# Kernel tuning notes

Measured on AMD Instinct MI355X. Metric: run time of the kernel, lower is better.

The kernel has to match this reference:

```python
import jax, jax.numpy as jnp
import numpy as np

D_MODEL = 2048
NUM_HEADS = 32
D_HEAD = D_MODEL // NUM_HEADS
L = 2048


def setup_inputs() -> dict:
    key = jax.random.key(0)
    ks = jax.random.split(key, 9)
    s = 0.02  # init scale
    return {
        "X": jax.random.normal(ks[0], (L, D_MODEL), dtype=jnp.float32),
        "Wq_w": jax.random.normal(ks[1], (D_MODEL, D_MODEL), jnp.float32) * s,
        "Wq_b": jax.random.normal(ks[2], (D_MODEL,), jnp.float32) * s,
        "Wk_w": jax.random.normal(ks[3], (D_MODEL, D_MODEL), jnp.float32) * s,
        "Wk_b": jax.random.normal(ks[4], (D_MODEL,), jnp.float32) * s,
        "Wv_w": jax.random.normal(ks[5], (D_MODEL, D_MODEL), jnp.float32) * s,
        "Wv_b": jax.random.normal(ks[6], (D_MODEL,), jnp.float32) * s,
        "Wo_w": jax.random.normal(ks[7], (D_MODEL, D_MODEL), jnp.float32) * s,
        "Wo_b": jax.random.normal(ks[8], (D_MODEL,), jnp.float32) * s,
    }


def reference(X, Wq_w, Wq_b, Wk_w, Wk_b, Wv_w, Wv_b, Wo_w, Wo_b):
    # torch.nn.Linear: y = x @ W.T + b
    seq = X.shape[0]
    Q = (X @ Wq_w.T + Wq_b).reshape(seq, D_HEAD, NUM_HEADS)  # (L, d, h)
    K = (X @ Wk_w.T + Wk_b).reshape(seq, D_HEAD, NUM_HEADS)
    V = (X @ Wv_w.T + Wv_b).reshape(seq, D_HEAD, NUM_HEADS)
    # scores[l, m, h] = sum_d Q[l,d,h] * K[m,d,h]; note scale is sqrt(d_model),
    # faithful to the source (not sqrt(d_head)).
    scores = jnp.einsum('ldh,mdh->lmh', Q, K) / jnp.sqrt(jnp.float32(D_MODEL))
    attn = jax.nn.softmax(scores, axis=1)  # softmax over key axis m
    out = jnp.einsum('lmh,mdh->ldh', attn, V).reshape(seq, D_MODEL)
    return out @ Wo_w.T + Wo_b
```

## Files before the change

kernel.cpp:

```cpp
#include <hip/hip_runtime.h>
#include <hip/hip_bf16.h>
#include <stdint.h>
#include <stddef.h>

#define L_SEQ   2048
#define DM      2048
#define NH      32
#define DH      64
#define QSCALE  0.02209708691207961f
#define QS2     0.0318793579f
#define MAT_N   (L_SEQ * DM)

typedef __bf16  bf16x8 __attribute__((ext_vector_type(8)));
typedef float   f32x4  __attribute__((ext_vector_type(4)));
typedef __hip_bfloat16 bf16;

#if __has_builtin(__builtin_amdgcn_exp2f)
#define EXP2F(x) __builtin_amdgcn_exp2f(x)
#else
#define EXP2F(x) __expf((x) * 0.6931471805599453f)
#endif

__device__ __forceinline__ void gl_lds16(const bf16* g, bf16* l) {
    __builtin_amdgcn_global_load_lds(
        (const __attribute__((address_space(1))) unsigned int*)g,
        (__attribute__((address_space(3))) unsigned int*)l,
        16, 0, 0);
}

__device__ __forceinline__ void conv8s(const float* src, bf16* dst, int i, float sc) {
    float4 a = *(const float4*)(src + i);
    float4 b = *(const float4*)(src + i + 4);
    union { bf16 h[8]; uint4 u; } pk;
    pk.h[0] = __float2bfloat16(a.x * sc); pk.h[1] = __float2bfloat16(a.y * sc);
    pk.h[2] = __float2bfloat16(a.z * sc); pk.h[3] = __float2bfloat16(a.w * sc);
    pk.h[4] = __float2bfloat16(b.x * sc); pk.h[5] = __float2bfloat16(b.y * sc);
    pk.h[6] = __float2bfloat16(b.z * sc); pk.h[7] = __float2bfloat16(b.w * sc);
    *(uint4*)(dst + i) = pk.u;
}

__global__ __launch_bounds__(256)
void convert4_kernel(const float* __restrict__ s0, const float* __restrict__ s1,
                     const float* __restrict__ s2, const float* __restrict__ s3,
                     bf16* __restrict__ d0, bf16* __restrict__ d1,
                     bf16* __restrict__ d2, bf16* __restrict__ d3)
{
    const float* s; bf16* d; float sc = 1.0f;
    switch (blockIdx.y) {
        case 0:  s = s0; d = d0; break;
        case 1:  s = s1; d = d1; sc = QS2; break;
        case 2:  s = s2; d = d2; break;
        default: s = s3; d = d3; break;
    }
    const int i = (blockIdx.x * 256 + threadIdx.x) * 8;
    conv8s(s, d, i, sc);
}

__global__ __launch_bounds__(256)
void convert_wo_perm_kernel(const float* __restrict__ s, bf16* __restrict__ d)
{
    const int t   = blockIdx.x * 256 + threadIdx.x;
    const int row = t >> 8;
    const int k0  = (t & 255) * 8;
    const float* sr = s + (size_t)row * DM;
    union { bf16 h[8]; uint4 u; } pk;
#pragma unroll
    for (int j = 0; j < 8; ++j) {
        const int kp = k0 + j;
        const int k  = ((kp & 63) << 5) | (kp >> 6);
        pk.h[j] = __float2bfloat16(sr[k]);
    }
    *(uint4*)(d + (size_t)row * DM + k0) = pk.u;
}

__global__ __launch_bounds__(512)
void qkv8_gemm_kernel(const bf16* __restrict__ Xb,
                      const bf16* __restrict__ Wq, const float* __restrict__ bq,
                      const bf16* __restrict__ Wk, const float* __restrict__ bk,
                      const bf16* __restrict__ Wv, const float* __restrict__ bv,
                      bf16* __restrict__ Qws, bf16* __restrict__ Kws, bf16* __restrict__ Vws,
                      const float* __restrict__ WoSrc, bf16* __restrict__ WobDst)
{
    __shared__ bf16 lds[2 * 32768];

    const int bid = blockIdx.x;
    const int tid  = threadIdx.x;

    if (bid >= 192) {
        const int t = (bid - 192) * 512 + tid;
        const int row = t >> 4;
        const int k0base = (t & 15) * 128;
        const float* sr = WoSrc + (size_t)row * DM;
        bf16* dr = WobDst + (size_t)row * DM;
        for (int i = 0; i < 16; ++i) {
            const int k0 = k0base + i * 8;
            union { bf16 h[8]; uint4 u; } pk;
#pragma unroll
            for (int j = 0; j < 8; ++j) {
                const int kp = k0 + j;
                const int k  = ((kp & 63) << 5) | (kp >> 6);
                pk.h[j] = __float2bfloat16(sr[k]);
            }
            *(uint4*)(dr + k0) = pk.u;
        }
        return;
    }

    const int mt  = bid & 7;
    const int nt  = bid >> 3;
    const int m0  = mt << 8;
    const int ng0 = nt << 8;
    const int z   = ng0 >> 11;
    const int n0  = ng0 & 2047;
    const bf16*  W    = (z == 0) ? Wq : (z == 1) ? Wk : Wv;
    const float* bias = (z == 0) ? bq : (z == 1) ? bk : bv;

    const int lane = tid & 63;
    const int wave = tid >> 6;
    const int wm   = wave >> 2;
    const int wn   = wave & 3;
    const int grp8 = (lane >> 4) * 8;
    const int grp4 = (lane >> 4) * 4;
    const int l15  = lane & 15;
    const int axor = (l15 & 7) << 3;

    const int scol = ((tid & 7) * 8) ^ (((tid >> 3) & 7) << 3);
    const bf16* gb[8];
    int loff[8];
#pragma unroll
    for (int e = 0; e < 8; ++e) {
        const int hh  = e >> 1;
        const int row = (e & 1) * 64 + (tid >> 3);
        loff[e] = hh * 8192 + (e & 1) * 4096 + tid * 8;
        if (hh < 2) {
            gb[e] = Xb + (size_t)(m0 + hh * 128 + row) * DM + scol;
        } else {
            const int nn   = n0 + (hh - 2) * 128 + row;
            const int brow = ((nn & 63) << 5) | (nn >> 6);
            gb[e] = W + (size_t)brow * DM + scol;
        }
    }

    const bool swap  = (z == 2);
    const int  aside = swap ? 16384 : 0;
    const int  bside = swap ? 0 : 16384;
    const bf16* fa0 = lds + aside + wm * 8192 + l15 * 64;
    const bf16* fb0 = lds + bside + (wn >> 1) * 8192 + ((wn & 1) * 64 + l15) * 64;

    f32x4 acc[8][4];
    const f32x4 zero = {0.f, 0.f, 0.f, 0.f};
#pragma unroll
    for (int i = 0; i < 8; ++i)
#pragma unroll
        for (int j = 0; j < 4; ++j) acc[i][j] = zero;

#pragma unroll
    for (int e = 0; e < 8; ++e) gl_lds16(gb[e],      lds + loff[e]);
#pragma unroll
    for (int e = 0; e < 8; ++e) gl_lds16(gb[e] + 64, lds + 32768 + loff[e]);
    asm volatile("s_waitcnt vmcnt(8)" ::: "memory");
    asm volatile("s_barrier" ::: "memory");

    for (int t = 0; t < 32; ++t) {
        const int cb = (t & 1) << 15;
        const bf16* fa = fa0 + cb;
        const bf16* fb = fb0 + cb;
        const int c0 = grp8 ^ axor;
        const int c1 = (32 + grp8) ^ axor;

        bf16x8 af[8], bfr[4];
#pragma unroll
        for (int i = 0; i < 8; ++i) af[i] = *(const bf16x8*)(fa + i * 1024 + c0);
#pragma unroll
        for (int j = 0; j < 4; ++j) bfr[j] = *(const bf16x8*)(fb + j * 1024 + c0);
        asm volatile("s_barrier" ::: "memory");
        __builtin_amdgcn_s_setprio(1);
#pragma unroll
        for (int i = 0; i < 8; ++i)
#pragma unroll
            for (int j = 0; j < 4; ++j)
                acc[i][j] = __builtin_amdgcn_mfma_f32_16x16x32_bf16(af[i], bfr[j], acc[i][j], 0, 0, 0);
        __builtin_amdgcn_s_setprio(0);

#pragma unroll
        for (int i = 0; i < 8; ++i) af[i] = *(const bf16x8*)(fa + i * 1024 + c1);
#pragma unroll
        for (int j = 0; j < 4; ++j) bfr[j] = *(const bf16x8*)(fb + j * 1024 + c1);
        asm volatile("s_waitcnt lgkmcnt(0)" ::: "memory");
        asm volatile("s_barrier" ::: "memory");
        if (t + 2 < 32) {
            const int kb2 = (t + 2) << 6;
#pragma unroll
            for (int e = 0; e < 8; ++e)
                gl_lds16(gb[e] + kb2, lds + cb + loff[e]);
            asm volatile("s_waitcnt vmcnt(8)" ::: "memory");
        } else if (t == 30) {
            asm volatile("s_waitcnt vmcnt(0)" ::: "memory");
        }
        __builtin_amdgcn_s_setprio(1);
#pragma unroll
        for (int i = 0; i < 8; ++i)
#pragma unroll
            for (int j = 0; j < 4; ++j)
                acc[i][j] = __builtin_amdgcn_mfma_f32_16x16x32_bf16(af[i], bfr[j], acc[i][j], 0, 0, 0);
        __builtin_amdgcn_s_setprio(0);
        asm volatile("s_barrier" ::: "memory");
    }

    if (z == 0) {
#pragma unroll
        for (int j = 0; j < 4; ++j) {
            const int np = n0 + wn * 64 + j * 16 + l15;
            const float bb = bias[((np & 63) << 5) | (np >> 6)] * QS2;
            const size_t base = ((size_t)(np >> 6) * L_SEQ) * DH + (np & 63);
#pragma unroll
            for (int i = 0; i < 8; ++i)
#pragma unroll
                for (int r = 0; r < 4; ++r) {
                    const int m = m0 + wm * 128 + i * 16 + grp4 + r;
                    Qws[base + (size_t)m * DH] = __float2bfloat16(acc[i][j][r] + bb);
                }
        }
    } else if (z == 1) {
#pragma unroll
        for (int j = 0; j < 4; ++j) {
            const int np = n0 + wn * 64 + j * 16 + l15;
            const float bb = bias[((np & 63) << 5) | (np >> 6)];
            const size_t base = ((size_t)(np >> 6) * L_SEQ) * DH + (np & 63);
#pragma unroll
            for (int i = 0; i < 8; ++i)
#pragma unroll
                for (int r = 0; r < 4; ++r) {
                    const int m = m0 + wm * 128 + i * 16 + grp4 + r;
                    Kws[base + (size_t)m * DH] = __float2bfloat16(acc[i][j][r] + bb);
                }
        }
    } else {
#pragma unroll
        for (int i = 0; i < 8; ++i)
#pragma unroll
            for (int r = 0; r < 4; ++r) {
                const int np = n0 + wm * 128 + i * 16 + grp4 + r;
                const float bb = bias[((np & 63) << 5) | (np >> 6)];
#pragma unroll
                for (int j = 0; j < 4; ++j) {
                    const int mcol = m0 + wn * 64 + j * 16 + l15;
                    Vws[(size_t)np * L_SEQ + mcol] = __float2bfloat16(acc[i][j][r] + bb);
                }
            }
    }
}

__global__ __launch_bounds__(512)
void out_fused_kernel(const bf16* __restrict__ A,
                      const bf16* __restrict__ Wo,
                      const float* __restrict__ bo,
                      float* __restrict__ out)
{
    __shared__ bf16 lds[2 * 16384];

    const int m0 = blockIdx.y * 128, n0 = blockIdx.x * 128;
    const int tid  = threadIdx.x;
    const int lane = tid & 63;
    const int wave = tid >> 6;
    const int wm   = wave >> 1;
    const int wn   = wave & 1;
    const int grp8 = (lane >> 4) * 8;
    const int grp4 = (lane >> 4) * 4;
    const int l15  = lane & 15;
    const int axor = (l15 & 7) << 3;

    const bf16* gb[4]; int loff[4];
#pragma unroll
    for (int e = 0; e < 4; ++e) {
        const int idx = (e & 1) * 512 + tid;
        const int row = idx >> 3;
        const int sc  = ((idx & 7) * 8) ^ ((row & 7) << 3);
        if (e < 2) { gb[e] = A  + (size_t)(m0 + row) * DM + sc; loff[e] = idx * 8; }
        else       { gb[e] = Wo + (size_t)(n0 + row) * DM + sc; loff[e] = 8192 + idx * 8; }
    }

    f32x4 acc[2][4];
    const f32x4 zero = {0.f, 0.f, 0.f, 0.f};
#pragma unroll
    for (int i = 0; i < 2; ++i)
#pragma unroll
        for (int j = 0; j < 4; ++j) acc[i][j] = zero;

#pragma unroll
    for (int e = 0; e < 4; ++e) gl_lds16(gb[e],      lds + loff[e]);
#pragma unroll
    for (int e = 0; e < 4; ++e) gl_lds16(gb[e] + 64, lds + 16384 + loff[e]);
    asm volatile("s_waitcnt vmcnt(4)" ::: "memory");
    asm volatile("s_barrier" ::: "memory");

    for (int t = 0; t < 32; ++t) {
        const int cb = (t & 1) << 14;
        const bf16* fa = lds + cb;
        const bf16* fb = lds + cb + 8192;
        const int c0 = grp8 ^ axor;
        const int c1 = (32 + grp8) ^ axor;

        bf16x8 af[2], bfr[4];
#pragma unroll
        for (int i = 0; i < 2; ++i) af[i]  = *(const bf16x8*)(fa + (wm * 32 + i * 16 + l15) * 64 + c0);
#pragma unroll
        for (int j = 0; j < 4; ++j) bfr[j] = *(const bf16x8*)(fb + (wn * 64 + j * 16 + l15) * 64 + c0);
        asm volatile("s_barrier" ::: "memory");
        __builtin_amdgcn_s_setprio(1);
#pragma unroll
        for (int i = 0; i < 2; ++i)
#pragma unroll
            for (int j = 0; j < 4; ++j)
                acc[i][j] = __builtin_amdgcn_mfma_f32_16x16x32_bf16(af[i], bfr[j], acc[i][j], 0, 0, 0);
        __builtin_amdgcn_s_setprio(0);

#pragma unroll
        for (int i = 0; i < 2; ++i) af[i]  = *(const bf16x8*)(fa + (wm * 32 + i * 16 + l15) * 64 + c1);
#pragma unroll
        for (int j = 0; j < 4; ++j) bfr[j] = *(const bf16x8*)(fb + (wn * 64 + j * 16 + l15) * 64 + c1);
        asm volatile("s_waitcnt lgkmcnt(0)" ::: "memory");
        asm volatile("s_barrier" ::: "memory");
        if (t + 2 < 32) {
            const int kadv = (t + 2) * 64;
#pragma unroll
            for (int e = 0; e < 4; ++e) gl_lds16(gb[e] + kadv, lds + cb + loff[e]);
            asm volatile("s_waitcnt vmcnt(4)" ::: "memory");
        } else if (t == 30) {
            asm volatile("s_waitcnt vmcnt(0)" ::: "memory");
        }
        __builtin_amdgcn_s_setprio(1);
#pragma unroll
        for (int i = 0; i < 2; ++i)
#pragma unroll
            for (int j = 0; j < 4; ++j)
                acc[i][j] = __builtin_amdgcn_mfma_f32_16x16x32_bf16(af[i], bfr[j], acc[i][j], 0, 0, 0);
        __builtin_amdgcn_s_setprio(0);
        asm volatile("s_barrier" ::: "memory");
    }

#pragma unroll
    for (int j = 0; j < 4; ++j) {
        const int n = n0 + wn * 64 + j * 16 + l15;
        const float bb = bo[n];
#pragma unroll
        for (int i = 0; i < 2; ++i) {
#pragma unroll
            for (int r = 0; r < 4; ++r) {
                const int m = m0 + wm * 32 + i * 16 + grp4 + r;
                out[(size_t)m * DM + n] = acc[i][j][r] + bb;
            }
        }
    }
}

__global__ __launch_bounds__(512)
void attention_kernel(const bf16* __restrict__ Qws,
                      const bf16* __restrict__ Kws,
                      const bf16* __restrict__ Vws,
                      bf16* __restrict__ Attn)
{
    __shared__ bf16 lds[24576];

    const int h = blockIdx.x, qb = blockIdx.y;
    const int tid  = threadIdx.x;
    const int wave = tid >> 6;
    const int lane = tid & 63;
    const int grp  = lane >> 4;
    const int l15  = lane & 15;
    const int grp8 = grp * 8;
    const int axor = (l15 & 7) << 3;

    const bf16* Qh = Qws + (size_t)h * L_SEQ * DH;
    const bf16* Kh = Kws + (size_t)h * L_SEQ * DH;
    const bf16* Vh = Vws + (size_t)h * DH * L_SEQ;

    const int q0 = qb * 128 + wave * 16;

    bf16x8 qf0 = *(const bf16x8*)(Qh + (size_t)(q0 + l15) * DH + grp8);
    bf16x8 qf1 = *(const bf16x8*)(Qh + (size_t)(q0 + l15) * DH + 32 + grp8);

    const int srow = tid >> 3;
    const int scol = ((tid & 7) * 8) ^ ((srow & 7) << 3);
    const bf16* gK = Kh + (size_t)srow * DH + scol;
    const bf16* gV = Vh + (size_t)srow * L_SEQ + scol;
    bf16* ldsK = lds + tid * 8;
    bf16* ldsV = lds + 8192 + tid * 8;
    bf16* Plds = lds + 16384;
    const int prow = (wave * 16 + l15) * 64;

    const f32x4 zero = {0.f, 0.f, 0.f, 0.f};
    f32x4 Oacc[4];
#pragma unroll
    for (int t = 0; t < 4; ++t) Oacc[t] = zero;
    float lsum = 0.f;

    gl_lds16(gK,        ldsK);
    gl_lds16(gV,        ldsV);
    gl_lds16(gK + 4096, ldsK + 4096);
    gl_lds16(gV + 64,   ldsV + 4096);
    asm volatile("s_waitcnt vmcnt(2)" ::: "memory");
    asm volatile("s_barrier" ::: "memory");

    for (int kb = 0; kb < 32; ++kb) {
        const int cb = (kb & 1) << 12;
        const bf16* Kc = lds + cb;
        const bf16* Vc = lds + 8192 + cb;

#pragma unroll
        for (int t = 0; t < 4; ++t) {
            const int rr = (t * 16 + l15) * 64;
            bf16x8 k0 = *(const bf16x8*)(Kc + rr + (grp8 ^ axor));
            bf16x8 k1 = *(const bf16x8*)(Kc + rr + ((32 + grp8) ^ axor));
            f32x4 s = zero;
            __builtin_amdgcn_s_setprio(1);
            s = __builtin_amdgcn_mfma_f32_16x16x32_bf16(k0, qf0, s, 0, 0, 0);
            s = __builtin_amdgcn_mfma_f32_16x16x32_bf16(k1, qf1, s, 0, 0, 0);
            __builtin_amdgcn_s_setprio(0);
            float p0 = EXP2F(s[0]), p1 = EXP2F(s[1]),
                  p2 = EXP2F(s[2]), p3 = EXP2F(s[3]);
            lsum += (p0 + p1) + (p2 + p3);
            union { bf16 hh[4]; uint2 u; } pk;
            pk.hh[0] = __float2bfloat16(p0); pk.hh[1] = __float2bfloat16(p1);
            pk.hh[2] = __float2bfloat16(p2); pk.hh[3] = __float2bfloat16(p3);
            *(uint2*)(&Plds[prow + ((t * 16 + grp * 4) ^ axor)]) = pk.u;
        }
        asm volatile("s_waitcnt lgkmcnt(0)" ::: "memory");

        __builtin_amdgcn_s_setprio(1);
#pragma unroll
        for (int ks = 0; ks < 2; ++ks) {
            bf16x8 pa = *(const bf16x8*)(&Plds[prow + ((ks * 32 + grp8) ^ axor)]);
#pragma unroll
            for (int t = 0; t < 4; ++t) {
                bf16x8 vb = *(const bf16x8*)(Vc + (t * 16 + l15) * 64 + ((ks * 32 + grp8) ^ axor));
                Oacc[t] = __builtin_amdgcn_mfma_f32_16x16x32_bf16(pa, vb, Oacc[t], 0, 0, 0);
            }
        }
        __builtin_amdgcn_s_setprio(0);

        asm volatile("s_waitcnt lgkmcnt(0)" ::: "memory");
        asm volatile("s_barrier" ::: "memory");
        if (kb + 2 < 32) {
            gl_lds16(gK + (kb + 2) * 4096, ldsK + cb);
            gl_lds16(gV + (kb + 2) * 64,   ldsV + cb);
            asm volatile("s_waitcnt vmcnt(2)" ::: "memory");
        } else if (kb == 30) {
            asm volatile("s_waitcnt vmcnt(0)" ::: "memory");
        }
        asm volatile("s_barrier" ::: "memory");
    }

    float sden = lsum;
    sden += __shfl_xor(sden, 16, 64);
    sden += __shfl_xor(sden, 32, 64);
    const float inv = 1.f / sden;
    float invs[4];
#pragma unroll
    for (int r = 0; r < 4; ++r)
        invs[r] = __shfl(inv, grp * 4 + r, 64);

#pragma unroll
    for (int t = 0; t < 4; ++t) {
#pragma unroll
        for (int r = 0; r < 4; ++r) {
            const int m = q0 + grp * 4 + r;
            const int d = t * 16 + l15;
            Attn[(size_t)m * DM + h * 64 + d] = __float2bfloat16(Oacc[t][r] * invs[r]);
        }
    }
}

extern "C" void kernel_launch(void* const* d_in, const int* in_sizes, int n_in,
                              void* d_out, int out_size, void* d_ws, size_t ws_size,
                              hipStream_t stream)
{
    const float* X  = (const float*)d_in[0];
    const float* Wq = (const float*)d_in[1];
    const float* bq = (const float*)d_in[2];
    const float* Wk = (const float*)d_in[3];
    const float* bk = (const float*)d_in[4];
    const float* Wv = (const float*)d_in[5];
    const float* bv = (const float*)d_in[6];
    const float* Wo = (const float*)d_in[7];
    const float* bo = (const float*)d_in[8];
    float* out = (float*)d_out;

    bf16* Xb   = (bf16*)d_ws;
    bf16* Wqb  = Xb  + (size_t)MAT_N;
    bf16* Wkb  = Wqb + (size_t)MAT_N;
    bf16* Wvb  = Wkb + (size_t)MAT_N;
    bf16* Qws  = Wvb + (size_t)MAT_N;
    bf16* Kws  = Qws + (size_t)MAT_N;
    bf16* Vws  = Kws + (size_t)MAT_N;
    bf16* Wob7 = Vws + (size_t)MAT_N;
    bf16* Attn = Wqb;

    const bool big = ws_size >= (size_t)8 * MAT_N * sizeof(bf16);
    bf16* Wob = big ? Wob7 : Xb;

    convert4_kernel<<<dim3(2048, 4), 256, 0, stream>>>(X, Wq, Wk, Wv, Xb, Wqb, Wkb, Wvb);
    if (big) {
        qkv8_gemm_kernel<<<dim3(256), 512, 0, stream>>>(Xb, Wqb, bq, Wkb, bk, Wvb, bv,
                                                        Qws, Kws, Vws, Wo, Wob7);
    } else {
        qkv8_gemm_kernel<<<dim3(192), 512, 0, stream>>>(Xb, Wqb, bq, Wkb, bk, Wvb, bv,
                                                        Qws, Kws, Vws, Wo, Wob);
        convert_wo_perm_kernel<<<dim3(2048), 256, 0, stream>>>(Wo, Wob);
    }
    attention_kernel<<<dim3(32, 16), 512, 0, stream>>>(Qws, Kws, Vws, Attn);
    out_fused_kernel<<<dim3(16, 16), 512, 0, stream>>>(Attn, Wob, bo, out);
}
```

Before: 249.7 us.

## Interleave QKV GEMM global prefetch across eight MFMA sub-phases and remap tile order

The QKV projection main loop is restructured into eight sub-phases per pair of K tiles. Each sub-phase issues a quarter of the next tile's global-to-LDS loads, so memory traffic is spread across the MFMA work rather than issued in one burst. The block-to-tile mapping is also changed so that consecutive blocks share M tiles in groups of three N tiles, aiming at better L2 reuse. In exchange the loop has many more barriers and lgkmcnt waits per tile, and the finer fragment reloads from LDS add synchronisation overhead.

```diff
diff --git a/kernel.cpp b/kernel.cpp
--- a/kernel.cpp
+++ b/kernel.cpp
@@ -20,6 +20,9 @@
 #else
 #define EXP2F(x) __expf((x) * 0.6931471805599453f)
 #endif
+
+#define BAR()   asm volatile("s_barrier" ::: "memory")
+#define LGKM0() asm volatile("s_waitcnt lgkmcnt(0)" ::: "memory")
 
 __device__ __forceinline__ void gl_lds16(const bf16* g, bf16* l) {
     __builtin_amdgcn_global_load_lds(
@@ -106,8 +109,10 @@
         return;
     }
 
-    const int mt  = bid & 7;
-    const int nt  = bid >> 3;
+    const int x   = bid & 7;
+    const int idx = bid >> 3;
+    const int mt  = idx / 3;
+    const int nt  = 3 * x + (idx - mt * 3);
     const int m0  = mt << 8;
     const int ng0 = nt << 8;
     const int z   = ng0 >> 11;
@@ -154,58 +159,109 @@
 #pragma unroll
         for (int j = 0; j < 4; ++j) acc[i][j] = zero;
 
+    const int c0 = grp8 ^ axor;
+    const int c1 = (32 + grp8) ^ axor;
+
+#define STAGE(hh, tile, bufoff) do { \
+        gl_lds16(gb[2*(hh)]     + (tile) * 64, lds + (bufoff) + loff[2*(hh)]); \
+        gl_lds16(gb[2*(hh) + 1] + (tile) * 64, lds + (bufoff) + loff[2*(hh)+1]); } while (0)
+
+#define MFMA16(BASE) do { \
+        __builtin_amdgcn_s_setprio(1); \
+        _Pragma("unroll") \
+        for (int i = 0; i < 4; ++i) \
+        _Pragma("unroll") \
+        for (int j = 0; j < 4; ++j) \
+            acc[(BASE) + i][j] = __builtin_amdgcn_mfma_f32_16x16x32_bf16(a[i], b[j], acc[(BASE) + i][j], 0, 0, 0); \
+        __builtin_amdgcn_s_setprio(0); } while (0)
+
 #pragma unroll
     for (int e = 0; e < 8; ++e) gl_lds16(gb[e],      lds + loff[e]);
 #pragma unroll
     for (int e = 0; e < 8; ++e) gl_lds16(gb[e] + 64, lds + 32768 + loff[e]);
     asm volatile("s_waitcnt vmcnt(8)" ::: "memory");
-    asm volatile("s_barrier" ::: "memory");
-
-    for (int t = 0; t < 32; ++t) {
-        const int cb = (t & 1) << 15;
-        const bf16* fa = fa0 + cb;
-        const bf16* fb = fb0 + cb;
-        const int c0 = grp8 ^ axor;
-        const int c1 = (32 + grp8) ^ axor;
-
-        bf16x8 af[8], bfr[4];
-#pragma unroll
-        for (int i = 0; i < 8; ++i) af[i] = *(const bf16x8*)(fa + i * 1024 + c0);
-#pragma unroll
-        for (int j = 0; j < 4; ++j) bfr[j] = *(const bf16x8*)(fb + j * 1024 + c0);
-        asm volatile("s_barrier" ::: "memory");
-        __builtin_amdgcn_s_setprio(1);
-#pragma unroll
-        for (int i = 0; i < 8; ++i)
-#pragma unroll
-            for (int j = 0; j < 4; ++j)
-                acc[i][j] = __builtin_amdgcn_mfma_f32_16x16x32_bf16(af[i], bfr[j], acc[i][j], 0, 0, 0);
-        __builtin_amdgcn_s_setprio(0);
-
-#pragma unroll
-        for (int i = 0; i < 8; ++i) af[i] = *(const bf16x8*)(fa + i * 1024 + c1);
-#pragma unroll
-        for (int j = 0; j < 4; ++j) bfr[j] = *(const bf16x8*)(fb + j * 1024 + c1);
-        asm volatile("s_waitcnt lgkmcnt(0)" ::: "memory");
-        asm volatile("s_barrier" ::: "memory");
-        if (t + 2 < 32) {
-            const int kb2 = (t + 2) << 6;
-#pragma unroll
-            for (int e = 0; e < 8; ++e)
-                gl_lds16(gb[e] + kb2, lds + cb + loff[e]);
-            asm volatile("s_waitcnt vmcnt(8)" ::: "memory");
-        } else if (t == 30) {
+    BAR();
+
+    for (int u = 0; u < 16; ++u) {
+        const int t0 = 2 * u;
+        const bf16* faA = fa0;           const bf16* fbA = fb0;
+        const bf16* faB = fa0 + 32768;   const bf16* fbB = fb0 + 32768;
+        bf16x8 a[4], b[4];
+
+#pragma unroll
+        for (int i = 0; i < 4; ++i) a[i] = *(const bf16x8*)(faA + i * 1024 + c0);
+#pragma unroll
+        for (int j = 0; j < 4; ++j) b[j] = *(const bf16x8*)(fbA + j * 1024 + c0);
+        if (u > 0) STAGE(1, t0 + 1, 32768);
+        BAR(); LGKM0();
+        MFMA16(0);
+        BAR();
+
+#pragma unroll
+        for (int i = 0; i < 4; ++i) a[i] = *(const bf16x8*)(faA + (4 + i) * 1024 + c0);
+        if (u > 0) STAGE(2, t0 + 1, 32768);
+        BAR(); LGKM0();
+        MFMA16(4);
+        BAR();
+
+#pragma unroll
+        for (int i = 0; i < 4; ++i) a[i] = *(const bf16x8*)(faA + i * 1024 + c1);
+#pragma unroll
+        for (int j = 0; j < 4; ++j) b[j] = *(const bf16x8*)(fbA + j * 1024 + c1);
+        if (u > 0) STAGE(3, t0 + 1, 32768);
+        BAR(); LGKM0();
+        MFMA16(0);
+        BAR();
+
+#pragma unroll
+        for (int i = 0; i < 4; ++i) a[i] = *(const bf16x8*)(faA + (4 + i) * 1024 + c1);
+        if (u < 15) {
+            STAGE(0, t0 + 2, 0);
+            asm volatile("s_waitcnt vmcnt(2)" ::: "memory");
+        } else {
             asm volatile("s_waitcnt vmcnt(0)" ::: "memory");
         }
-        __builtin_amdgcn_s_setprio(1);
-#pragma unroll
-        for (int i = 0; i < 8; ++i)
-#pragma unroll
-            for (int j = 0; j < 4; ++j)
-                acc[i][j] = __builtin_amdgcn_mfma_f32_16x16x32_bf16(af[i], bfr[j], acc[i][j], 0, 0, 0);
-        __builtin_amdgcn_s_setprio(0);
-        asm volatile("s_barrier" ::: "memory");
-    }
+        BAR(); LGKM0();
+        MFMA16(4);
+        BAR();
+
+#pragma unroll
+        for (int i = 0; i < 4; ++i) a[i] = *(const bf16x8*)(faB + i * 1024 + c0);
+#pragma unroll
+        for (int j = 0; j < 4; ++j) b[j] = *(const bf16x8*)(fbB + j * 1024 + c0);
+        if (u < 15) STAGE(1, t0 + 2, 0);
+        BAR(); LGKM0();
+        MFMA16(0);
+        BAR();
+
+#pragma unroll
+        for (int i = 0; i < 4; ++i) a[i] = *(const bf16x8*)(faB + (4 + i) * 1024 + c0);
+        if (u < 15) STAGE(2, t0 + 2, 0);
+        BAR(); LGKM0();
+        MFMA16(4);
+        BAR();
+
+#pragma unroll
+        for (int i = 0; i < 4; ++i) a[i] = *(const bf16x8*)(faB + i * 1024 + c1);
+#pragma unroll
+        for (int j = 0; j < 4; ++j) b[j] = *(const bf16x8*)(fbB + j * 1024 + c1);
+        if (u < 15) STAGE(3, t0 + 2, 0);
+        BAR(); LGKM0();
+        MFMA16(0);
+        BAR();
+
+#pragma unroll
+        for (int i = 0; i < 4; ++i) a[i] = *(const bf16x8*)(faB + (4 + i) * 1024 + c1);
+        if (u < 15) {
+            STAGE(0, t0 + 3, 32768);
+            asm volatile("s_waitcnt vmcnt(2)" ::: "memory");
+        }
+        BAR(); LGKM0();
+        MFMA16(4);
+        BAR();
+    }
+#undef STAGE
+#undef MFMA16
 
     if (z == 0) {
 #pragma unroll
@@ -292,7 +348,7 @@
 #pragma unroll
     for (int e = 0; e < 4; ++e) gl_lds16(gb[e] + 64, lds + 16384 + loff[e]);
     asm volatile("s_waitcnt vmcnt(4)" ::: "memory");
-    asm volatile("s_barrier" ::: "memory");
+    BAR();
 
     for (int t = 0; t < 32; ++t) {
         const int cb = (t & 1) << 14;
@@ -306,7 +362,7 @@
         for (int i = 0; i < 2; ++i) af[i]  = *(const bf16x8*)(fa + (wm * 32 + i * 16 + l15) * 64 + c0);
 #pragma unroll
         for (int j = 0; j < 4; ++j) bfr[j] = *(const bf16x8*)(fb + (wn * 64 + j * 16 + l15) * 64 + c0);
-        asm volatile("s_barrier" ::: "memory");
+        BAR();
         __builtin_amdgcn_s_setprio(1);
 #pragma unroll
         for (int i = 0; i < 2; ++i)
@@ -319,8 +375,8 @@
         for (int i = 0; i < 2; ++i) af[i]  = *(const bf16x8*)(fa + (wm * 32 + i * 16 + l15) * 64 + c1);
 #pragma unroll
         for (int j = 0; j < 4; ++j) bfr[j] = *(const bf16x8*)(fb + (wn * 64 + j * 16 + l15) * 64 + c1);
-        asm volatile("s_waitcnt lgkmcnt(0)" ::: "memory");
-        asm volatile("s_barrier" ::: "memory");
+        LGKM0();
+        BAR();
         if (t + 2 < 32) {
             const int kadv = (t + 2) * 64;
 #pragma unroll
@@ -336,7 +392,7 @@
             for (int j = 0; j < 4; ++j)
                 acc[i][j] = __builtin_amdgcn_mfma_f32_16x16x32_bf16(af[i], bfr[j], acc[i][j], 0, 0, 0);
         __builtin_amdgcn_s_setprio(0);
-        asm volatile("s_barrier" ::: "memory");
+        BAR();
     }
 
 #pragma unroll
@@ -400,7 +456,7 @@
     gl_lds16(gK + 4096, ldsK + 4096);
     gl_lds16(gV + 64,   ldsV + 4096);
     asm volatile("s_waitcnt vmcnt(2)" ::: "memory");
-    asm volatile("s_barrier" ::: "memory");
+    BAR();
 
     for (int kb = 0; kb < 32; ++kb) {
         const int cb = (kb & 1) << 12;
@@ -425,7 +481,7 @@
             pk.hh[2] = __float2bfloat16(p2); pk.hh[3] = __float2bfloat16(p3);
             *(uint2*)(&Plds[prow + ((t * 16 + grp * 4) ^ axor)]) = pk.u;
         }
-        asm volatile("s_waitcnt lgkmcnt(0)" ::: "memory");
+        LGKM0();
 
         __builtin_amdgcn_s_setprio(1);
 #pragma unroll
@@ -439,8 +495,8 @@
         }
         __builtin_amdgcn_s_setprio(0);
 
-        asm volatile("s_waitcnt lgkmcnt(0)" ::: "memory");
-        asm volatile("s_barrier" ::: "memory");
+        LGKM0();
+        BAR();
         if (kb + 2 < 32) {
             gl_lds16(gK + (kb + 2) * 4096, ldsK + cb);
             gl_lds16(gV + (kb + 2) * 64,   ldsV + cb);
@@ -448,7 +504,7 @@
         } else if (kb == 30) {
             asm volatile("s_waitcnt vmcnt(0)" ::: "memory");
         }
-        asm volatile("s_barrier" ::: "memory");
+        BAR();
     }
 
     float sden = lsum;
```

Measured after the change: 248.9 us. Within noise of the previous version (-0.3%).

## Fuse all stages into one cooperative persistent kernel with grid syncs

Applied to the files above, without the earlier changes.

Replaces the four separate launches (convert, QKV GEMM, attention, output GEMM) with a single cooperative kernel of 256 blocks that runs each stage and separates them with grid.sync. The attention stage now processes two query blocks per workgroup and uses a 4-deep K/V LDS ring in place of a 2-deep one, loading two key tiles per barrier pair. This aims to remove launch gaps and inter-kernel drain/fill overhead. In exchange it adds grid-wide barriers, fixes the grid at 256 blocks of 512 threads (possibly lower occupancy in the convert and attention stages), and raises LDS use, falling back to the old path if the cooperative launch fails.

```diff
diff --git a/kernel.cpp b/kernel.cpp
--- a/kernel.cpp
+++ b/kernel.cpp
@@ -1,7 +1,10 @@
 #include <hip/hip_runtime.h>
+#include <hip/hip_cooperative_groups.h>
 #include <hip/hip_bf16.h>
 #include <stdint.h>
 #include <stddef.h>
+
+namespace cg = cooperative_groups;
 
 #define L_SEQ   2048
 #define DM      2048
@@ -39,53 +42,14 @@
     *(uint4*)(dst + i) = pk.u;
 }
 
-__global__ __launch_bounds__(256)
-void convert4_kernel(const float* __restrict__ s0, const float* __restrict__ s1,
-                     const float* __restrict__ s2, const float* __restrict__ s3,
-                     bf16* __restrict__ d0, bf16* __restrict__ d1,
-                     bf16* __restrict__ d2, bf16* __restrict__ d3)
-{
-    const float* s; bf16* d; float sc = 1.0f;
-    switch (blockIdx.y) {
-        case 0:  s = s0; d = d0; break;
-        case 1:  s = s1; d = d1; sc = QS2; break;
-        case 2:  s = s2; d = d2; break;
-        default: s = s3; d = d3; break;
-    }
-    const int i = (blockIdx.x * 256 + threadIdx.x) * 8;
-    conv8s(s, d, i, sc);
-}
-
-__global__ __launch_bounds__(256)
-void convert_wo_perm_kernel(const float* __restrict__ s, bf16* __restrict__ d)
-{
-    const int t   = blockIdx.x * 256 + threadIdx.x;
-    const int row = t >> 8;
-    const int k0  = (t & 255) * 8;
-    const float* sr = s + (size_t)row * DM;
-    union { bf16 h[8]; uint4 u; } pk;
-#pragma unroll
-    for (int j = 0; j < 8; ++j) {
-        const int kp = k0 + j;
-        const int k  = ((kp & 63) << 5) | (kp >> 6);
-        pk.h[j] = __float2bfloat16(sr[k]);
-    }
-    *(uint4*)(d + (size_t)row * DM + k0) = pk.u;
-}
-
-__global__ __launch_bounds__(512)
-void qkv8_gemm_kernel(const bf16* __restrict__ Xb,
-                      const bf16* __restrict__ Wq, const float* __restrict__ bq,
-                      const bf16* __restrict__ Wk, const float* __restrict__ bk,
-                      const bf16* __restrict__ Wv, const float* __restrict__ bv,
-                      bf16* __restrict__ Qws, bf16* __restrict__ Kws, bf16* __restrict__ Vws,
-                      const float* __restrict__ WoSrc, bf16* __restrict__ WobDst)
-{
-    __shared__ bf16 lds[2 * 32768];
-
-    const int bid = blockIdx.x;
-    const int tid  = threadIdx.x;
-
+__device__ void qkv_stage(bf16* lds, int bid, int tid,
+                          const bf16* __restrict__ Xb,
+                          const bf16* __restrict__ Wq, const float* __restrict__ bq,
+                          const bf16* __restrict__ Wk, const float* __restrict__ bk,
+                          const bf16* __restrict__ Wv, const float* __restrict__ bv,
+                          bf16* __restrict__ Qws, bf16* __restrict__ Kws, bf16* __restrict__ Vws,
+                          const float* __restrict__ WoSrc, bf16* __restrict__ WobDst)
+{
     if (bid >= 192) {
         const int t = (bid - 192) * 512 + tid;
         const int row = t >> 4;
@@ -251,16 +215,127 @@
     }
 }
 
-__global__ __launch_bounds__(512)
-void out_fused_kernel(const bf16* __restrict__ A,
-                      const bf16* __restrict__ Wo,
-                      const float* __restrict__ bo,
-                      float* __restrict__ out)
-{
-    __shared__ bf16 lds[2 * 16384];
-
-    const int m0 = blockIdx.y * 128, n0 = blockIdx.x * 128;
-    const int tid  = threadIdx.x;
+__device__ void attention_stage(bf16* lds, int h, int qb, int tid,
+                                const bf16* __restrict__ Qws, const bf16* __restrict__ Kws,
+                                const bf16* __restrict__ Vws, bf16* __restrict__ Attn)
+{
+    const int wave = tid >> 6;
+    const int lane = tid & 63;
+    const int grp  = lane >> 4;
+    const int l15  = lane & 15;
+    const int grp8 = grp * 8;
+    const int axor = (l15 & 7) << 3;
+
+    const bf16* Qh = Qws + (size_t)h * L_SEQ * DH;
+    const bf16* Kh = Kws + (size_t)h * L_SEQ * DH;
+    const bf16* Vh = Vws + (size_t)h * DH * L_SEQ;
+
+    const int q0 = qb * 128 + wave * 16;
+
+    bf16x8 qf0 = *(const bf16x8*)(Qh + (size_t)(q0 + l15) * DH + grp8);
+    bf16x8 qf1 = *(const bf16x8*)(Qh + (size_t)(q0 + l15) * DH + 32 + grp8);
+
+    const int srow = tid >> 3;
+    const int scol = ((tid & 7) * 8) ^ ((srow & 7) << 3);
+    const bf16* gK = Kh + (size_t)srow * DH + scol;
+    const bf16* gV = Vh + (size_t)srow * L_SEQ + scol;
+    bf16* Plds = lds + 32768;
+    const int prow = (wave * 16 + l15) * 64;
+
+    const f32x4 zero = {0.f, 0.f, 0.f, 0.f};
+    f32x4 Oacc[4];
+#pragma unroll
+    for (int t = 0; t < 4; ++t) Oacc[t] = zero;
+    float lsum = 0.f;
+
+#pragma unroll
+    for (int s = 0; s < 4; ++s) {
+        gl_lds16(gK + s * 4096, lds + s * 4096 + tid * 8);
+        gl_lds16(gV + s * 64,   lds + 16384 + s * 4096 + tid * 8);
+    }
+    asm volatile("s_waitcnt vmcnt(4)" ::: "memory");
+    asm volatile("s_barrier" ::: "memory");
+
+    for (int i = 0; i < 16; ++i) {
+#pragma unroll
+        for (int half = 0; half < 2; ++half) {
+            const int u  = 2 * i + half;
+            const bf16* Kc = lds + (u & 3) * 4096;
+            const bf16* Vc = lds + 16384 + (u & 3) * 4096;
+
+#pragma unroll
+            for (int t = 0; t < 4; ++t) {
+                const int rr = (t * 16 + l15) * 64;
+                bf16x8 k0 = *(const bf16x8*)(Kc + rr + (grp8 ^ axor));
+                bf16x8 k1 = *(const bf16x8*)(Kc + rr + ((32 + grp8) ^ axor));
+                f32x4 s = zero;
+                __builtin_amdgcn_s_setprio(1);
+                s = __builtin_amdgcn_mfma_f32_16x16x32_bf16(k0, qf0, s, 0, 0, 0);
+                s = __builtin_amdgcn_mfma_f32_16x16x32_bf16(k1, qf1, s, 0, 0, 0);
+                __builtin_amdgcn_s_setprio(0);
+                float p0 = EXP2F(s[0]), p1 = EXP2F(s[1]),
+                      p2 = EXP2F(s[2]), p3 = EXP2F(s[3]);
+                lsum += (p0 + p1) + (p2 + p3);
+                union { bf16 hh[4]; uint2 u2; } pk;
+                pk.hh[0] = __float2bfloat16(p0); pk.hh[1] = __float2bfloat16(p1);
+                pk.hh[2] = __float2bfloat16(p2); pk.hh[3] = __float2bfloat16(p3);
+                *(uint2*)(&Plds[prow + ((t * 16 + grp * 4) ^ axor)]) = pk.u2;
+            }
+            asm volatile("s_waitcnt lgkmcnt(0)" ::: "memory");
+
+            __builtin_amdgcn_s_setprio(1);
+#pragma unroll
+            for (int ks = 0; ks < 2; ++ks) {
+                bf16x8 pa = *(const bf16x8*)(&Plds[prow + ((ks * 32 + grp8) ^ axor)]);
+#pragma unroll
+                for (int t = 0; t < 4; ++t) {
+                    bf16x8 vb = *(const bf16x8*)(Vc + (t * 16 + l15) * 64 + ((ks * 32 + grp8) ^ axor));
+                    Oacc[t] = __builtin_amdgcn_mfma_f32_16x16x32_bf16(pa, vb, Oacc[t], 0, 0, 0);
+                }
+            }
+            __builtin_amdgcn_s_setprio(0);
+            asm volatile("s_waitcnt lgkmcnt(0)" ::: "memory");
+        }
+
+        asm volatile("s_barrier" ::: "memory");
+        if (i + 2 < 16) {
+            const int u2 = 2 * i + 4;
+#pragma unroll
+            for (int s = 0; s < 2; ++s) {
+                gl_lds16(gK + (size_t)(u2 + s) * 4096, lds + ((u2 + s) & 3) * 4096 + tid * 8);
+                gl_lds16(gV + (u2 + s) * 64,           lds + 16384 + ((u2 + s) & 3) * 4096 + tid * 8);
+            }
+            asm volatile("s_waitcnt vmcnt(4)" ::: "memory");
+        } else if (i == 14) {
+            asm volatile("s_waitcnt vmcnt(0)" ::: "memory");
+        }
+        asm volatile("s_barrier" ::: "memory");
+    }
+
+    float sden = lsum;
+    sden += __shfl_xor(sden, 16, 64);
+    sden += __shfl_xor(sden, 32, 64);
+    const float inv = 1.f / sden;
+    float invs[4];
+#pragma unroll
+    for (int r = 0; r < 4; ++r)
+        invs[r] = __shfl(inv, grp * 4 + r, 64);
+
+#pragma unroll
+    for (int t = 0; t < 4; ++t) {
+#pragma unroll
+        for (int r = 0; r < 4; ++r) {
+            const int m = q0 + grp * 4 + r;
+            const int d = t * 16 + l15;
+            Attn[(size_t)m * DM + h * 64 + d] = __float2bfloat16(Oacc[t][r] * invs[r]);
+        }
+    }
+}
+
+__device__ void out_stage(bf16* lds, int m0, int n0, int tid,
+                          const bf16* __restrict__ A, const bf16* __restrict__ Wo,
+                          const float* __restrict__ bo, float* __restrict__ out)
+{
     const int lane = tid & 63;
     const int wave = tid >> 6;
     const int wm   = wave >> 1;
@@ -355,120 +430,106 @@
 }
 
 __global__ __launch_bounds__(512)
-void attention_kernel(const bf16* __restrict__ Qws,
-                      const bf16* __restrict__ Kws,
-                      const bf16* __restrict__ Vws,
-                      bf16* __restrict__ Attn)
-{
-    __shared__ bf16 lds[24576];
-
-    const int h = blockIdx.x, qb = blockIdx.y;
-    const int tid  = threadIdx.x;
-    const int wave = tid >> 6;
-    const int lane = tid & 63;
-    const int grp  = lane >> 4;
-    const int l15  = lane & 15;
-    const int grp8 = grp * 8;
-    const int axor = (l15 & 7) << 3;
-
-    const bf16* Qh = Qws + (size_t)h * L_SEQ * DH;
-    const bf16* Kh = Kws + (size_t)h * L_SEQ * DH;
-    const bf16* Vh = Vws + (size_t)h * DH * L_SEQ;
-
-    const int q0 = qb * 128 + wave * 16;
-
-    bf16x8 qf0 = *(const bf16x8*)(Qh + (size_t)(q0 + l15) * DH + grp8);
-    bf16x8 qf1 = *(const bf16x8*)(Qh + (size_t)(q0 + l15) * DH + 32 + grp8);
-
-    const int srow = tid >> 3;
-    const int scol = ((tid & 7) * 8) ^ ((srow & 7) << 3);
-    const bf16* gK = Kh + (size_t)srow * DH + scol;
-    const bf16* gV = Vh + (size_t)srow * L_SEQ + scol;
-    bf16* ldsK = lds + tid * 8;
-    bf16* ldsV = lds + 8192 + tid * 8;
-    bf16* Plds = lds + 16384;
-    const int prow = (wave * 16 + l15) * 64;
-
-    const f32x4 zero = {0.f, 0.f, 0.f, 0.f};
-    f32x4 Oacc[4];
-#pragma unroll
-    for (int t = 0; t < 4; ++t) Oacc[t] = zero;
-    float lsum = 0.f;
-
-    gl_lds16(gK,        ldsK);
-    gl_lds16(gV,        ldsV);
-    gl_lds16(gK + 4096, ldsK + 4096);
-    gl_lds16(gV + 64,   ldsV + 4096);
-    asm volatile("s_waitcnt vmcnt(2)" ::: "memory");
-    asm volatile("s_barrier" ::: "memory");
-
-    for (int kb = 0; kb < 32; ++kb) {
-        const int cb = (kb & 1) << 12;
-        const bf16* Kc = lds + cb;
-        const bf16* Vc = lds + 8192 + cb;
-
-#pragma unroll
-        for (int t = 0; t < 4; ++t) {
-            const int rr = (t * 16 + l15) * 64;
-            bf16x8 k0 = *(const bf16x8*)(Kc + rr + (grp8 ^ axor));
-            bf16x8 k1 = *(const bf16x8*)(Kc + rr + ((32 + grp8) ^ axor));
-            f32x4 s = zero;
-            __builtin_amdgcn_s_setprio(1);
-            s = __builtin_amdgcn_mfma_f32_16x16x32_bf16(k0, qf0, s, 0, 0, 0);
-            s = __builtin_amdgcn_mfma_f32_16x16x32_bf16(k1, qf1, s, 0, 0, 0);
-            __builtin_amdgcn_s_setprio(0);
-            float p0 = EXP2F(s[0]), p1 = EXP2F(s[1]),
-                  p2 = EXP2F(s[2]), p3 = EXP2F(s[3]);
-            lsum += (p0 + p1) + (p2 + p3);
-            union { bf16 hh[4]; uint2 u; } pk;
-            pk.hh[0] = __float2bfloat16(p0); pk.hh[1] = __float2bfloat16(p1);
-            pk.hh[2] = __float2bfloat16(p2); pk.hh[3] = __float2bfloat16(p3);
-            *(uint2*)(&Plds[prow + ((t * 16 + grp * 4) ^ axor)]) = pk.u;
-        }
-        asm volatile("s_waitcnt lgkmcnt(0)" ::: "memory");
-
-        __builtin_amdgcn_s_setprio(1);
-#pragma unroll
-        for (int ks = 0; ks < 2; ++ks) {
-            bf16x8 pa = *(const bf16x8*)(&Plds[prow + ((ks * 32 + grp8) ^ axor)]);
-#pragma unroll
-            for (int t = 0; t < 4; ++t) {
-                bf16x8 vb = *(const bf16x8*)(Vc + (t * 16 + l15) * 64 + ((ks * 32 + grp8) ^ axor));
-                Oacc[t] = __builtin_amdgcn_mfma_f32_16x16x32_bf16(pa, vb, Oacc[t], 0, 0, 0);
-            }
-        }
-        __builtin_amdgcn_s_setprio(0);
-
-        asm volatile("s_waitcnt lgkmcnt(0)" ::: "memory");
-        asm volatile("s_barrier" ::: "memory");
-        if (kb + 2 < 32) {
-            gl_lds16(gK + (kb + 2) * 4096, ldsK + cb);
-            gl_lds16(gV + (kb + 2) * 64,   ldsV + cb);
-            asm volatile("s_waitcnt vmcnt(2)" ::: "memory");
-        } else if (kb == 30) {
-            asm volatile("s_waitcnt vmcnt(0)" ::: "memory");
-        }
-        asm volatile("s_barrier" ::: "memory");
-    }
-
-    float sden = lsum;
-    sden += __shfl_xor(sden, 16, 64);
-    sden += __shfl_xor(sden, 32, 64);
-    const float inv = 1.f / sden;
-    float invs[4];
-#pragma unroll
-    for (int r = 0; r < 4; ++r)
-        invs[r] = __shfl(inv, grp * 4 + r, 64);
-
-#pragma unroll
-    for (int t = 0; t < 4; ++t) {
-#pragma unroll
-        for (int r = 0; r < 4; ++r) {
-            const int m = q0 + grp * 4 + r;
-            const int d = t * 16 + l15;
-            Attn[(size_t)m * DM + h * 64 + d] = __float2bfloat16(Oacc[t][r] * invs[r]);
-        }
-    }
+void mha_mega_kernel(const float* __restrict__ X,
+                     const float* __restrict__ Wq, const float* __restrict__ bq,
+                     const float* __restrict__ Wk, const float* __restrict__ bk,
+                     const float* __restrict__ Wv, const float* __restrict__ bv,
+                     const float* __restrict__ Wo, const float* __restrict__ bo,
+                     bf16* Xb, bf16* Wqb, bf16* Wkb, bf16* Wvb,
+                     bf16* Qws, bf16* Kws, bf16* Vws, bf16* Wob, bf16* Attn,
+                     float* out)
+{
+    __shared__ bf16 lds[2 * 32768];
+    cg::grid_group grid = cg::this_grid();
+    const int bid = blockIdx.x;
+    const int tid = threadIdx.x;
+
+    {
+        const int G = bid * 512 + tid;
+#pragma unroll
+        for (int j = 0; j < 4; ++j) {
+            const int i = (j * 131072 + G) * 8;
+            conv8s(X,  Xb,  i, 1.0f);
+            conv8s(Wq, Wqb, i, QS2);
+            conv8s(Wk, Wkb, i, 1.0f);
+            conv8s(Wv, Wvb, i, 1.0f);
+        }
+    }
+    __threadfence();
+    grid.sync();
+
+    qkv_stage(lds, bid, tid, Xb, Wqb, bq, Wkb, bk, Wvb, bv, Qws, Kws, Vws, Wo, Wob);
+    __threadfence();
+    grid.sync();
+
+    attention_stage(lds, bid & 31, bid >> 5,       tid, Qws, Kws, Vws, Attn);
+    attention_stage(lds, bid & 31, (bid >> 5) + 8, tid, Qws, Kws, Vws, Attn);
+    __threadfence();
+    grid.sync();
+
+    out_stage(lds, (bid >> 4) * 128, (bid & 15) * 128, tid, Attn, Wob, bo, out);
+}
+
+__global__ __launch_bounds__(256)
+void convert4_kernel(const float* __restrict__ s0, const float* __restrict__ s1,
+                     const float* __restrict__ s2, const float* __restrict__ s3,
+                     bf16* __restrict__ d0, bf16* __restrict__ d1,
+                     bf16* __restrict__ d2, bf16* __restrict__ d3)
+{
+    const float* s; bf16* d; float sc = 1.0f;
+    switch (blockIdx.y) {
+        case 0:  s = s0; d = d0; break;
+        case 1:  s = s1; d = d1; sc = QS2; break;
+        case 2:  s = s2; d = d2; break;
+        default: s = s3; d = d3; break;
+    }
+    const int i = (blockIdx.x * 256 + threadIdx.x) * 8;
+    conv8s(s, d, i, sc);
+}
+
+__global__ __launch_bounds__(256)
+void convert_wo_perm_kernel(const float* __restrict__ s, bf16* __restrict__ d)
+{
+    const int t   = blockIdx.x * 256 + threadIdx.x;
+    const int row = t >> 8;
+    const int k0  = (t & 255) * 8;
+    const float* sr = s + (size_t)row * DM;
+    union { bf16 h[8]; uint4 u; } pk;
+#pragma unroll
+    for (int j = 0; j < 8; ++j) {
+        const int kp = k0 + j;
+        const int k  = ((kp & 63) << 5) | (kp >> 6);
+        pk.h[j] = __float2bfloat16(sr[k]);
+    }
+    *(uint4*)(d + (size_t)row * DM + k0) = pk.u;
+}
+
+__global__ __launch_bounds__(512)
+void qkv8_gemm_kernel(const bf16* __restrict__ Xb,
+                      const bf16* __restrict__ Wq, const float* __restrict__ bq,
+                      const bf16* __restrict__ Wk, const float* __restrict__ bk,
+                      const bf16* __restrict__ Wv, const float* __restrict__ bv,
+                      bf16* __restrict__ Qws, bf16* __restrict__ Kws, bf16* __restrict__ Vws,
+                      const float* __restrict__ WoSrc, bf16* __restrict__ WobDst)
+{
+    __shared__ bf16 lds[2 * 32768];
+    qkv_stage(lds, blockIdx.x, threadIdx.x, Xb, Wq, bq, Wk, bk, Wv, bv, Qws, Kws, Vws, WoSrc, WobDst);
+}
+
+__global__ __launch_bounds__(512)
+void attention_kernel(const bf16* __restrict__ Qws, const bf16* __restrict__ Kws,
+                      const bf16* __restrict__ Vws, bf16* __restrict__ Attn)
+{
+    __shared__ bf16 lds[40960];
+    attention_stage(lds, blockIdx.x, blockIdx.y, threadIdx.x, Qws, Kws, Vws, Attn);
+}
+
+__global__ __launch_bounds__(512)
+void out_fused_kernel(const bf16* __restrict__ A, const bf16* __restrict__ Wo,
+                      const float* __restrict__ bo, float* __restrict__ out)
+{
+    __shared__ bf16 lds[2 * 16384];
+    out_stage(lds, blockIdx.y * 128, blockIdx.x * 128, threadIdx.x, A, Wo, bo, out);
 }
 
 extern "C" void kernel_launch(void* const* d_in, const int* in_sizes, int n_in,
@@ -497,8 +558,21 @@
     bf16* Attn = Wqb;
 
     const bool big = ws_size >= (size_t)8 * MAT_N * sizeof(bf16);
+
+    if (big) {
+        void* args[] = {
+            (void*)&X, (void*)&Wq, (void*)&bq, (void*)&Wk, (void*)&bk,
+            (void*)&Wv, (void*)&bv, (void*)&Wo, (void*)&bo,
+            (void*)&Xb, (void*)&Wqb, (void*)&Wkb, (void*)&Wvb,
+            (void*)&Qws, (void*)&Kws, (void*)&Vws, (void*)&Wob7, (void*)&Attn,
+            (void*)&out
+        };
+        hipError_t e = hipLaunchCooperativeKernel((const void*)mha_mega_kernel,
+                                                  dim3(256), dim3(512), args, 0, stream);
+        if (e == hipSuccess) return;
+    }
+
     bf16* Wob = big ? Wob7 : Xb;
-
     convert4_kernel<<<dim3(2048, 4), 256, 0, stream>>>(X, Wq, Wk, Wv, Xb, Wqb, Wkb, Wvb);
     if (big) {
         qkv8_gemm_kernel<<<dim3(256), 512, 0, stream>>>(Xb, Wqb, bq, Wkb, bk, Wvb, bv,
```

Result: slower. 609.3 us (+144.0%).
